# Kernel optimization log

Measured on AMD Instinct MI355X. Metric: run time of the kernel, lower is better.

## Reference

```python
import jax, jax.numpy as jnp
import numpy as np

NUM_NODES = 8192
IN_FEATURES = 1024
OUT_FEATURES = 512
NUM_EDGES = 262144  # avg degree 32


def setup_inputs() -> dict:
    key = jax.random.key(0)
    k_x, k_w, k_b, k_src, k_dst = jax.random.split(key, 5)
    x = jax.random.normal(k_x, (NUM_NODES, IN_FEATURES), dtype=jnp.float32)
    # torch nn.Linear layout: weight [out, in], bias [out]
    W = jax.random.normal(k_w, (OUT_FEATURES, IN_FEATURES), dtype=jnp.float32) * (1.0 / np.sqrt(IN_FEATURES))
    b = jax.random.normal(k_b, (OUT_FEATURES,), dtype=jnp.float32) * 0.01
    src = jax.random.randint(k_src, (NUM_EDGES,), 0, NUM_NODES, dtype=jnp.int64)
    dst = jax.random.randint(k_dst, (NUM_EDGES,), 0, NUM_NODES, dtype=jnp.int64)
    edge_index = jnp.stack([src, dst], axis=0)
    return {"x": x, "W": W, "b": b, "edge_index": edge_index, "num_nodes": NUM_NODES}


def reference(x, W, b, edge_index, num_nodes):
    # Faithful to the torch module: build dense adjacency from edge list
    # (duplicate edges collapse to 1.0 via assignment semantics),
    # linear, (dropout p=0 -> identity), dense adj @ hidden, relu.
    adj = jnp.zeros((num_nodes, num_nodes), dtype=x.dtype)
    adj = adj.at[edge_index[0], edge_index[1]].set(1.0)
    hidden = x @ W.T + b            # [N, out]
    support = adj @ hidden          # [N, out] aggregation over neighbors
    return jax.nn.relu(support)
```

## Files before the change

### kernel.cpp

```cpp
#include <hip/hip_runtime.h>

#define N_NODES 8192
#define IN_F    1024
#define OUT_F   512
#define N_EDGES 262144
#define STRIDE  96

#define HID_OFF     0u
#define WB_OFF      8388608u
#define DEG_OFF     9437184u
#define COL_OFF     9469952u
#define MAX_DEG     STRIDE

typedef short  bf16x8 __attribute__((ext_vector_type(8)));
typedef float  f32x4  __attribute__((ext_vector_type(4)));

__device__ __forceinline__ unsigned f2bf(float f) {
    unsigned u = __float_as_uint(f);
    u += 0x7fffu + ((u >> 16) & 1u);
    return u >> 16;
}

__device__ __forceinline__ float bflo(unsigned u) { return __uint_as_float(u << 16); }
__device__ __forceinline__ float bfhi(unsigned u) { return __uint_as_float(u & 0xffff0000u); }

__device__ __forceinline__ void ld_lds16(const void* g, void* l) {
    __builtin_amdgcn_global_load_lds(
        (const __attribute__((address_space(1))) void*)g,
        (__attribute__((address_space(3))) void*)l, 16, 0, 0);
}

#define NW8 (OUT_F * IN_F / 8)
__global__ __launch_bounds__(256) void prep(const float* __restrict__ w,
                                            unsigned short* __restrict__ wb,
                                            int* __restrict__ deg) {
    int i = blockIdx.x * blockDim.x + threadIdx.x;
    if (i < N_NODES) deg[i] = 0;
    const f32x4* p = (const f32x4*)w + (size_t)i * 2;
    f32x4 v0 = __builtin_nontemporal_load(p);
    f32x4 v1 = __builtin_nontemporal_load(p + 1);
    uint4 o;
    o.x = f2bf(v0.x) | (f2bf(v0.y) << 16);
    o.y = f2bf(v0.z) | (f2bf(v0.w) << 16);
    o.z = f2bf(v1.x) | (f2bf(v1.y) << 16);
    o.w = f2bf(v1.z) | (f2bf(v1.w) << 16);
    *((uint4*)wb + i) = o;
}

__global__ __launch_bounds__(256, 6) void gemm_scatter(const float* __restrict__ X,
                                                       const unsigned short* __restrict__ Wb,
                                                       const float* __restrict__ bias,
                                                       unsigned short* __restrict__ H,
                                                       const int* __restrict__ src,
                                                       const int* __restrict__ dst,
                                                       int* __restrict__ deg,
                                                       int* __restrict__ col) {
    __shared__ unsigned short As[64 * 64];
    __shared__ unsigned short Bs[64 * 64];

    const int bid = blockIdx.x;
    const int tid = threadIdx.x;

    if (bid >= 1024) {
        int e = (bid - 1024) * 256 + tid;
        int s = src[e];
        int slot = atomicAdd(&deg[s], 1);
        if (slot < STRIDE) col[s * STRIDE + slot] = dst[e];
        return;
    }

    const int lane = tid & 63;
    const int wave = tid >> 6;
    const int row0 = (bid & 127) * 64;
    const int col0 = (bid >> 7) * 64;
    const int wm   = (wave & 1) * 32;
    const int wn   = (wave >> 1) * 32;
    const int fm   = lane & 15;
    const int fm7  = fm & 7;
    const int q    = lane >> 4;

    f32x4 acc[2][2];
#pragma unroll
    for (int i = 0; i < 2; ++i)
#pragma unroll
        for (int j = 0; j < 2; ++j) acc[i][j] = (f32x4)0.f;

    const int ar   = tid >> 2;
    const int ak4  = tid & 3;
    const int ar7  = ar & 7;
    unsigned short* As_w0 = As + ar * 64 + ((ak4 * 2)     ^ ar7) * 8;
    unsigned short* As_w1 = As + ar * 64 + ((ak4 * 2 + 1) ^ ar7) * 8;
    const float* xrow = &X[(size_t)(row0 + ar) * IN_F + ak4 * 16];

    const int br = tid >> 3;
    const int bk = ((tid & 7) ^ (br & 7)) * 8;

    for (int k0 = 0; k0 < IN_F; k0 += 64) {
        const f32x4* px = (const f32x4*)(xrow + k0);
        f32x4 v0 = px[0], v1 = px[1], v2 = px[2], v3 = px[3];
        ld_lds16(Wb + (size_t)(col0 + br) * IN_F + k0 + bk,      Bs + tid * 8);
        ld_lds16(Wb + (size_t)(col0 + br + 32) * IN_F + k0 + bk, Bs + (tid + 256) * 8);
        uint4 pa, pb;
        pa.x = f2bf(v0.x) | (f2bf(v0.y) << 16);
        pa.y = f2bf(v0.z) | (f2bf(v0.w) << 16);
        pa.z = f2bf(v1.x) | (f2bf(v1.y) << 16);
        pa.w = f2bf(v1.z) | (f2bf(v1.w) << 16);
        pb.x = f2bf(v2.x) | (f2bf(v2.y) << 16);
        pb.y = f2bf(v2.z) | (f2bf(v2.w) << 16);
        pb.z = f2bf(v3.x) | (f2bf(v3.y) << 16);
        pb.w = f2bf(v3.z) | (f2bf(v3.w) << 16);
        *(uint4*)As_w0 = pa;
        *(uint4*)As_w1 = pb;
        __syncthreads();

#pragma unroll
        for (int s = 0; s < 2; ++s) {
            const int kq = s * 4 + q;
            bf16x8 a[2], b[2];
#pragma unroll
            for (int mi = 0; mi < 2; ++mi)
                a[mi] = *(const bf16x8*)&As[(((wm + mi * 16 + fm) << 3) + (kq ^ fm7)) << 3];
#pragma unroll
            for (int ni = 0; ni < 2; ++ni)
                b[ni] = *(const bf16x8*)&Bs[(((wn + ni * 16 + fm) << 3) + (kq ^ fm7)) << 3];
#pragma unroll
            for (int mi = 0; mi < 2; ++mi)
#pragma unroll
                for (int ni = 0; ni < 2; ++ni)
                    acc[mi][ni] = __builtin_amdgcn_mfma_f32_16x16x32_bf16(
                        a[mi], b[ni], acc[mi][ni], 0, 0, 0);
        }
        __syncthreads();
    }

    const int cm = (lane >> 4) * 4;
#pragma unroll
    for (int ni = 0; ni < 2; ++ni) {
        const int c = col0 + wn + ni * 16 + fm;
        const float bv = bias[c];
#pragma unroll
        for (int mi = 0; mi < 2; ++mi) {
#pragma unroll
            for (int r = 0; r < 4; ++r) {
                const int row = row0 + wm + mi * 16 + cm + r;
                H[(size_t)row * OUT_F + c] = (unsigned short)f2bf(acc[mi][ni][r] + bv);
            }
        }
    }
}

__global__ __launch_bounds__(256) void aggregate(const unsigned short* __restrict__ H,
                                                 const int* __restrict__ dg,
                                                 const int* __restrict__ col,
                                                 float* __restrict__ out) {
    __shared__ int nbr[4][MAX_DEG];
    __shared__ int uniq[4][MAX_DEG];
    __shared__ int wcnt[4];
    const int wave = threadIdx.x >> 6;
    const int lane = threadIdx.x & 63;
    const int v    = blockIdx.x * 4 + wave;
    int d = dg[v];
    if (d > MAX_DEG) d = MAX_DEG;

    if (lane == 0) wcnt[wave] = 0;
    int id0 = -1, id1 = -1;
    if (lane < d)      { id0 = col[v * STRIDE + lane];      nbr[wave][lane]      = id0; }
    if (64 + lane < d) { id1 = col[v * STRIDE + 64 + lane]; nbr[wave][64 + lane] = id1; }
    __builtin_amdgcn_wave_barrier();

    bool k0 = (lane < d);
    const int lim0 = k0 ? lane : 0;
    for (int j = 0; j < lim0; ++j) k0 = k0 & (nbr[wave][j] != id0);
    bool k1 = (64 + lane < d);
    const int lim1 = k1 ? (64 + lane) : 0;
    for (int j = 0; j < lim1; ++j) k1 = k1 & (nbr[wave][j] != id1);
    if (k0) uniq[wave][atomicAdd(&wcnt[wave], 1)] = id0;
    if (k1) uniq[wave][atomicAdd(&wcnt[wave], 1)] = id1;
    __builtin_amdgcn_wave_barrier();
    const int n  = wcnt[wave];
    const int f0 = lane * 8;

    float a0=0,a1=0,a2=0,a3=0,a4=0,a5=0,a6=0,a7=0;
    int e = 0;
    for (; e + 4 <= n; e += 4) {
        const int i0 = uniq[wave][e], i1 = uniq[wave][e+1],
                  i2 = uniq[wave][e+2], i3 = uniq[wave][e+3];
        uint4 h0 = *(const uint4*)&H[(size_t)i0 * OUT_F + f0];
        uint4 h1 = *(const uint4*)&H[(size_t)i1 * OUT_F + f0];
        uint4 h2 = *(const uint4*)&H[(size_t)i2 * OUT_F + f0];
        uint4 h3 = *(const uint4*)&H[(size_t)i3 * OUT_F + f0];
        a0 += bflo(h0.x)+bflo(h1.x)+bflo(h2.x)+bflo(h3.x);
        a1 += bfhi(h0.x)+bfhi(h1.x)+bfhi(h2.x)+bfhi(h3.x);
        a2 += bflo(h0.y)+bflo(h1.y)+bflo(h2.y)+bflo(h3.y);
        a3 += bfhi(h0.y)+bfhi(h1.y)+bfhi(h2.y)+bfhi(h3.y);
        a4 += bflo(h0.z)+bflo(h1.z)+bflo(h2.z)+bflo(h3.z);
        a5 += bfhi(h0.z)+bfhi(h1.z)+bfhi(h2.z)+bfhi(h3.z);
        a6 += bflo(h0.w)+bflo(h1.w)+bflo(h2.w)+bflo(h3.w);
        a7 += bfhi(h0.w)+bfhi(h1.w)+bfhi(h2.w)+bfhi(h3.w);
    }
    for (; e < n; ++e) {
        uint4 h0 = *(const uint4*)&H[(size_t)uniq[wave][e] * OUT_F + f0];
        a0 += bflo(h0.x); a1 += bfhi(h0.x);
        a2 += bflo(h0.y); a3 += bfhi(h0.y);
        a4 += bflo(h0.z); a5 += bfhi(h0.z);
        a6 += bflo(h0.w); a7 += bfhi(h0.w);
    }
    f32x4 o0 = {fmaxf(a0,0.f), fmaxf(a1,0.f), fmaxf(a2,0.f), fmaxf(a3,0.f)};
    f32x4 o1 = {fmaxf(a4,0.f), fmaxf(a5,0.f), fmaxf(a6,0.f), fmaxf(a7,0.f)};
    __builtin_nontemporal_store(o0, (f32x4*)&out[(size_t)v * OUT_F + f0]);
    __builtin_nontemporal_store(o1, (f32x4*)&out[(size_t)v * OUT_F + f0 + 4]);
}

extern "C" void kernel_launch(void* const* d_in, const int* in_sizes, int n_in,
                              void* d_out, int out_size, void* d_ws, size_t ws_size,
                              hipStream_t stream) {
    const float* x  = (const float*)d_in[0];
    const float* W  = (const float*)d_in[1];
    const float* b  = (const float*)d_in[2];
    const int*   ei = (const int*)d_in[3];
    float* out = (float*)d_out;

    char* ws = (char*)d_ws;
    unsigned short* H   = (unsigned short*)(ws + HID_OFF);
    unsigned short* Wb  = (unsigned short*)(ws + WB_OFF);
    int*            deg = (int*)(ws + DEG_OFF);
    int*            col = (int*)(ws + COL_OFF);

    prep<<<NW8 / 256, 256, 0, stream>>>(W, Wb, deg);

    gemm_scatter<<<2048, 256, 0, stream>>>(x, Wb, b, H, ei, ei + N_EDGES, deg, col);

    aggregate<<<N_NODES / 4, 256, 0, stream>>>(H, deg, col, out);
}
```

Baseline: 141.7 us.

## Build adjacency lists with per-block LDS histograms and scan instead of global atomics

Replaces the global-atomic scatter that was fused into the GEMM launch with three small kernels. The first builds a per-block source histogram in LDS, the second does a column-wise scan to get per-block offsets and degrees, and the third places destination indices using LDS atomics. The aim is to remove contended global atomics and to make the column order within each row deterministic. In exchange it adds three kernel launches, each running only 32 blocks, and these run serially before the GEMM instead of overlapping with it.

```diff
diff --git a/kernel.cpp b/kernel.cpp
--- a/kernel.cpp
+++ b/kernel.cpp
@@ -5,11 +5,14 @@
 #define OUT_F   512
 #define N_EDGES 262144
 #define STRIDE  96
+#define NBLK    32
 
 #define HID_OFF     0u
 #define WB_OFF      8388608u
 #define DEG_OFF     9437184u
 #define COL_OFF     9469952u
+#define BH_OFF      12615680u
+#define BO_OFF      13664256u
 #define MAX_DEG     STRIDE
 
 typedef short  bf16x8 __attribute__((ext_vector_type(8)));
@@ -32,10 +35,8 @@
 
 #define NW8 (OUT_F * IN_F / 8)
 __global__ __launch_bounds__(256) void prep(const float* __restrict__ w,
-                                            unsigned short* __restrict__ wb,
-                                            int* __restrict__ deg) {
+                                            unsigned short* __restrict__ wb) {
     int i = blockIdx.x * blockDim.x + threadIdx.x;
-    if (i < N_NODES) deg[i] = 0;
     const f32x4* p = (const f32x4*)w + (size_t)i * 2;
     f32x4 v0 = __builtin_nontemporal_load(p);
     f32x4 v1 = __builtin_nontemporal_load(p + 1);
@@ -47,28 +48,64 @@
     *((uint4*)wb + i) = o;
 }
 
-__global__ __launch_bounds__(256, 6) void gemm_scatter(const float* __restrict__ X,
-                                                       const unsigned short* __restrict__ Wb,
-                                                       const float* __restrict__ bias,
-                                                       unsigned short* __restrict__ H,
-                                                       const int* __restrict__ src,
-                                                       const int* __restrict__ dst,
-                                                       int* __restrict__ deg,
-                                                       int* __restrict__ col) {
+__global__ __launch_bounds__(256) void hist_a(const int* __restrict__ src,
+                                              int* __restrict__ blkhist) {
+    __shared__ int h[N_NODES];
+    const int b   = blockIdx.x;
+    const int tid = threadIdx.x;
+    for (int i = tid; i < N_NODES; i += 256) h[i] = 0;
+    __syncthreads();
+    const int e0 = b * (N_EDGES / NBLK);
+#pragma unroll
+    for (int j = 0; j < N_EDGES / NBLK / 256; ++j)
+        atomicAdd(&h[src[e0 + j * 256 + tid]], 1);
+    __syncthreads();
+    for (int i = tid; i < N_NODES; i += 256)
+        blkhist[b * N_NODES + i] = h[i];
+}
+
+__global__ __launch_bounds__(256) void scan_b(const int* __restrict__ blkhist,
+                                              int* __restrict__ boff,
+                                              int* __restrict__ deg) {
+    const int i = blockIdx.x * 256 + threadIdx.x;
+    int s = 0;
+#pragma unroll
+    for (int b = 0; b < NBLK; ++b) {
+        int t = blkhist[b * N_NODES + i];
+        boff[b * N_NODES + i] = s;
+        s += t;
+    }
+    deg[i] = s;
+}
+
+__global__ __launch_bounds__(256) void place_c(const int* __restrict__ src,
+                                               const int* __restrict__ dst,
+                                               const int* __restrict__ boff,
+                                               int* __restrict__ col) {
+    __shared__ int h[N_NODES];
+    const int b   = blockIdx.x;
+    const int tid = threadIdx.x;
+    for (int i = tid; i < N_NODES; i += 256) h[i] = 0;
+    __syncthreads();
+    const int e0 = b * (N_EDGES / NBLK);
+#pragma unroll
+    for (int j = 0; j < N_EDGES / NBLK / 256; ++j) {
+        int e = e0 + j * 256 + tid;
+        int s = src[e];
+        int r = boff[b * N_NODES + s] + atomicAdd(&h[s], 1);
+        if (r < STRIDE) col[s * STRIDE + r] = dst[e];
+    }
+}
+
+__global__ __launch_bounds__(256, 6) void gemm_mfma(const float* __restrict__ X,
+                                                    const unsigned short* __restrict__ Wb,
+                                                    const float* __restrict__ bias,
+                                                    unsigned short* __restrict__ H) {
     __shared__ unsigned short As[64 * 64];
     __shared__ unsigned short Bs[64 * 64];
 
-    const int bid = blockIdx.x;
-    const int tid = threadIdx.x;
-
-    if (bid >= 1024) {
-        int e = (bid - 1024) * 256 + tid;
-        int s = src[e];
-        int slot = atomicAdd(&deg[s], 1);
-        if (slot < STRIDE) col[s * STRIDE + slot] = dst[e];
-        return;
-    }
-
+    const int bid  = blockIdx.x;
+    const int tid  = threadIdx.x;
     const int lane = tid & 63;
     const int wave = tid >> 6;
     const int row0 = (bid & 127) * 64;
@@ -221,14 +258,20 @@
     float* out = (float*)d_out;
 
     char* ws = (char*)d_ws;
-    unsigned short* H   = (unsigned short*)(ws + HID_OFF);
-    unsigned short* Wb  = (unsigned short*)(ws + WB_OFF);
-    int*            deg = (int*)(ws + DEG_OFF);
-    int*            col = (int*)(ws + COL_OFF);
-
-    prep<<<NW8 / 256, 256, 0, stream>>>(W, Wb, deg);
-
-    gemm_scatter<<<2048, 256, 0, stream>>>(x, Wb, b, H, ei, ei + N_EDGES, deg, col);
-
+    unsigned short* H       = (unsigned short*)(ws + HID_OFF);
+    unsigned short* Wb      = (unsigned short*)(ws + WB_OFF);
+    int*            deg     = (int*)(ws + DEG_OFF);
+    int*            col     = (int*)(ws + COL_OFF);
+    int*            blkhist = (int*)(ws + BH_OFF);
+    int*            boff    = (int*)(ws + BO_OFF);
+
+    const int* src = ei;
+    const int* dst = ei + N_EDGES;
+
+    prep<<<NW8 / 256, 256, 0, stream>>>(W, Wb);
+    hist_a<<<NBLK, 256, 0, stream>>>(src, blkhist);
+    scan_b<<<N_NODES / 256, 256, 0, stream>>>(blkhist, boff, deg);
+    place_c<<<NBLK, 256, 0, stream>>>(src, dst, boff, col);
+    gemm_mfma<<<1024, 256, 0, stream>>>(x, Wb, b, H);
     aggregate<<<N_NODES / 4, 256, 0, stream>>>(H, deg, col, out);
 }
```

Measured after the change: 168.8 us. 19.1% more time.
